# Kernel optimization log

Measured on AMD Instinct MI355X. Metric: run time of the kernel, lower is better.

## Reference

```python
import jax, jax.numpy as jnp
import numpy as np
from jax import lax

B, L = 8192, 64
N_VALUES, EMBED, HIDDEN, OUT = 1000, 64, 128, 128


def setup_inputs() -> dict:
    key = jax.random.key(0)
    ks = jax.random.split(key, 8)
    s = 0.1  # weight scale ~ 1/sqrt(hidden)
    return {
        "x": jax.random.randint(ks[0], (B, L), 0, N_VALUES),
        "embed": jax.random.normal(ks[1], (N_VALUES, EMBED), jnp.float32) * s,
        "W_ih": jax.random.normal(ks[2], (3 * HIDDEN, EMBED), jnp.float32) * s,
        "W_hh": jax.random.normal(ks[3], (3 * HIDDEN, HIDDEN), jnp.float32) * s,
        "b_ih": jax.random.normal(ks[4], (3 * HIDDEN,), jnp.float32) * s,
        "b_hh": jax.random.normal(ks[5], (3 * HIDDEN,), jnp.float32) * s,
        "W_out": jax.random.normal(ks[6], (OUT, HIDDEN), jnp.float32) * s,
        "b_out": jax.random.normal(ks[7], (OUT,), jnp.float32) * s,
    }


def _gru_encode(x, embed, W_ih, W_hh, b_ih, b_hh, W_out, b_out):
    e = embed[x]  # [B, L, E] embedding lookup
    H = W_hh.shape[1]
    # Precompute input-to-gate projections for all timesteps (batched GEMM).
    xg = jnp.einsum('ble,ge->blg', e, W_ih) + b_ih  # [B, L, 3H]

    def step(h, xg_t):
        hg = h @ W_hh.T + b_hh  # [B, 3H]
        xr, xz, xn = jnp.split(xg_t, 3, axis=-1)
        hr, hz, hn = jnp.split(hg, 3, axis=-1)
        r = jax.nn.sigmoid(xr + hr)
        z = jax.nn.sigmoid(xz + hz)
        n = jnp.tanh(xn + r * hn)  # PyTorch GRU: r gates the hidden 'new' term
        h_new = (1.0 - z) * n + z * h
        return h_new, None

    h0 = jnp.zeros((x.shape[0], H), e.dtype)
    h_last, _ = lax.scan(step, h0, jnp.swapaxes(xg, 0, 1))  # scan over time
    return h_last @ W_out.T + b_out  # [B, OUT]


def reference(x, embed, W_ih, W_hh, b_ih, b_hh, W_out, b_out):
    return _gru_encode(x, embed, W_ih, W_hh, b_ih, b_hh, W_out, b_out)
```

## Files before the change

kernel.cpp:

```cpp
#include <hip/hip_runtime.h>


typedef __bf16 bf16x8 __attribute__((ext_vector_type(8)));
typedef float  f32x4  __attribute__((ext_vector_type(4)));
typedef int    int4v  __attribute__((ext_vector_type(4)));
typedef unsigned int uint2v __attribute__((ext_vector_type(2)));

#define NV   1000
#define EMB  64
#define HD   128
#define G3   384
#define SEQ  64
#define BB   16

#define SC_RZ (-1.4426950408889634f)
#define SC_N  ( 2.8853900817779268f)

__device__ __forceinline__ float bflo(unsigned int word) {
    return __builtin_bit_cast(float, word << 16);
}
__device__ __forceinline__ float bfhi(unsigned int word) {
    return __builtin_bit_cast(float, word & 0xffff0000u);
}

__global__ void g_table_kernel(const float* __restrict__ embed,
                               const float* __restrict__ W_ih,
                               const float* __restrict__ b_ih,
                               const float* __restrict__ b_hh,
                               unsigned short* __restrict__ Gpk)
{
    __shared__ float emb[EMB];
    const int v = blockIdx.x;
    const int g = threadIdx.x;
    if (g < EMB) emb[g] = embed[v * EMB + g];
    __syncthreads();
    const float* wr = W_ih + g * EMB;
    float s = b_ih[g] + (g < 2 * HD ? b_hh[g] : 0.f);
    #pragma unroll
    for (int e = 0; e < EMB; e += 4) {
        const float4 w4 = *(const float4*)(wr + e);
        s += w4.x * emb[e] + w4.y * emb[e + 1] + w4.z * emb[e + 2] + w4.w * emb[e + 3];
    }
    const int hid = g & 127, gate = g >> 7;
    s *= (gate < 2) ? SC_RZ : SC_N;
    const int w8 = hid >> 4, c16i = hid & 15;
    Gpk[((v * 8 + w8) * 16 + c16i) * 4 + gate] =
        __builtin_bit_cast(unsigned short, (__bf16)s);
}

#define GRU_STEP(P, T)                                                             \
  {                                                                                \
    int4v tk = {0, 0, 0, 0};                                                       \
    if ((T) < SEQ - 1) tk = *(const int4v*)&xl[((T) + 1) * BB + quad * 4];         \
    f32x4 acc[3];                                                                  \
    float xn_[4];                                                                  \
    _Pragma("unroll") for (int j = 0; j < 4; ++j) {                                \
      acc[0][j] = bflo(pf[j][0]);                                         \
      acc[1][j] = bfhi(pf[j][0]);                                         \
      acc[2][j] = bnw;                                                    \
      xn_[j]    = bflo(pf[j][1]);                                         \
    }                                                                              \
    _Pragma("unroll") for (int ks = 0; ks < 4; ++ks) {                             \
      const bf16x8 af = *(const bf16x8*)(hbase + (P) * 4096 + aoff[ks]);           \
      _Pragma("unroll") for (int gate = 0; gate < 3; ++gate)                       \
        acc[gate] = __builtin_amdgcn_mfma_f32_16x16x32_bf16(                       \
            af, wf[gate][ks], acc[gate], 0, 0, 0);                                 \
    }                                                                              \
    if ((T) < SEQ - 1) {                                                           \
      _Pragma("unroll") for (int j = 0; j < 4; ++j)                                \
        pf[j] = *(const uint2v*)(gbase + (unsigned)(tk[j] * 1024 + goff));         \
    }                                                                              \
    _Pragma("unroll") for (int j = 0; j < 4; ++j) {                                \
      const float r  = __builtin_amdgcn_rcpf(                                      \
          1.f + __builtin_amdgcn_exp2f(acc[0][j]));                                \
      const float zg = __builtin_amdgcn_rcpf(                                      \
          1.f + __builtin_amdgcn_exp2f(acc[1][j]));                                \
      const float v  = __builtin_fmaf(r, acc[2][j], xn_[j]);                       \
      const float n  = __builtin_fmaf(-2.f,                                        \
          __builtin_amdgcn_rcpf(1.f + __builtin_amdgcn_exp2f(v)), 1.f);            \
      const float hn = __builtin_fmaf(zg, hreg[j] - n, n);                         \
      hreg[j] = hn;                                                                \
      *(unsigned short*)(hbase + (1 - (P)) * 4096 + woff[j]) =                     \
          __builtin_bit_cast(unsigned short, (__bf16)hn);                          \
    }                                                                              \
    asm volatile("s_waitcnt lgkmcnt(0)" ::: "memory");                             \
    __builtin_amdgcn_s_barrier();                                                  \
    __builtin_amdgcn_sched_barrier(0);                                             \
  }

__global__ __launch_bounds__(512, 4) void gru_kernel(
    const int*   __restrict__ x,    const unsigned short* __restrict__ Gpk,
    const float* __restrict__ Whh,  const float* __restrict__ bhh,
    const float* __restrict__ Wout, const float* __restrict__ bout,
    float* __restrict__ out)
{
    __shared__ unsigned short hA[2 * BB * HD];
    __shared__ int xl[SEQ * BB];

    const int tid  = threadIdx.x;
    const int lane = tid & 63;
    const int w    = tid >> 6;
    const int c16  = lane & 15;
    const int quad = lane >> 4;
    const int br0  = blockIdx.x * BB;

    #pragma unroll
    for (int i = 0; i < 2; ++i) {
        const int idx = i * 512 + tid;
        const int r = idx >> 6;
        const int t = idx & 63;
        xl[t * BB + r] = x[(br0 + r) * SEQ + t];
    }
    {
        unsigned int* hA32 = (unsigned int*)hA;
        #pragma unroll
        for (int i = 0; i < 2; ++i)
            hA32[i * 512 + tid] = 0u;
    }

    bf16x8 wf[3][4];
    #pragma unroll
    for (int gate = 0; gate < 3; ++gate)
    #pragma unroll
    for (int ks = 0; ks < 4; ++ks) {
        const float sc = (gate < 2) ? SC_RZ : SC_N;
        const int col = gate * HD + w * 16 + c16;
        const float* p = Whh + col * HD + ks * 32 + quad * 4;
        const float4 a = *(const float4*)p;
        const float4 b = *(const float4*)(p + 16);
        bf16x8 f;
        f[0] = (__bf16)(sc * a.x); f[1] = (__bf16)(sc * a.y);
        f[2] = (__bf16)(sc * a.z); f[3] = (__bf16)(sc * a.w);
        f[4] = (__bf16)(sc * b.x); f[5] = (__bf16)(sc * b.y);
        f[6] = (__bf16)(sc * b.z); f[7] = (__bf16)(sc * b.w);
        wf[gate][ks] = f;
    }

    const float bnw = SC_N * bhh[2 * HD + w * 16 + c16];

    int aoff[4];
    #pragma unroll
    for (int ks = 0; ks < 4; ++ks)
        aoff[ks] = c16 * 256 + ((ks * 64 + quad * 16) ^ ((c16 & 7) << 4));
    int woff[4];
    {
        const int hid  = w * 16 + c16;
        const int sidx = ((hid >> 5) << 5) | (((hid & 15) >> 2) << 3)
                       | (((hid >> 4) & 1) << 2) | (hid & 3);
        #pragma unroll
        for (int j = 0; j < 4; ++j) {
            const int row = quad * 4 + j;
            woff[j] = row * 256 + ((sidx * 2) ^ ((row & 7) << 4));
        }
    }

    char* hbase = (char*)hA;
    const char* gbase = (const char*)Gpk;
    const int goff = w * 128 + c16 * 8;

    float hreg[4] = {0.f, 0.f, 0.f, 0.f};
    const f32x4 z4 = {0.f, 0.f, 0.f, 0.f};

    __syncthreads();

    uint2v pf[4];
    {
        const int4v tk0 = *(const int4v*)&xl[0 * BB + quad * 4];
        #pragma unroll
        for (int j = 0; j < 4; ++j)
            pf[j] = *(const uint2v*)(gbase + (unsigned)(tk0[j] * 1024 + goff));
    }

    for (int tt = 0; tt < SEQ; tt += 2) {
        GRU_STEP(0, tt);
        GRU_STEP(1, tt + 1);
    }

    bf16x8 wo[4];
    #pragma unroll
    for (int ks = 0; ks < 4; ++ks) {
        const int col = w * 16 + c16;
        const float* p = Wout + col * HD + ks * 32 + quad * 4;
        const float4 a = *(const float4*)p;
        const float4 b = *(const float4*)(p + 16);
        bf16x8 f;
        f[0] = (__bf16)a.x; f[1] = (__bf16)a.y; f[2] = (__bf16)a.z; f[3] = (__bf16)a.w;
        f[4] = (__bf16)b.x; f[5] = (__bf16)b.y; f[6] = (__bf16)b.z; f[7] = (__bf16)b.w;
        wo[ks] = f;
    }
    const float bow = bout[w * 16 + c16];

    f32x4 oacc = z4;
    #pragma unroll
    for (int ks = 0; ks < 4; ++ks) {
        const bf16x8 af = *(const bf16x8*)(hbase + aoff[ks]);
        oacc = __builtin_amdgcn_mfma_f32_16x16x32_bf16(af, wo[ks], oacc, 0, 0, 0);
    }
    #pragma unroll
    for (int j = 0; j < 4; ++j) {
        const int row = br0 + quad * 4 + j;
        out[row * HD + w * 16 + c16] = oacc[j] + bow;
    }
}

extern "C" void kernel_launch(void* const* d_in, const int* in_sizes, int n_in,
                              void* d_out, int out_size, void* d_ws, size_t ws_size,
                              hipStream_t stream) {
    const int*   x     = (const int*)  d_in[0];
    const float* embed = (const float*)d_in[1];
    const float* W_ih  = (const float*)d_in[2];
    const float* W_hh  = (const float*)d_in[3];
    const float* b_ih  = (const float*)d_in[4];
    const float* b_hh  = (const float*)d_in[5];
    const float* W_out = (const float*)d_in[6];
    const float* b_out = (const float*)d_in[7];
    float* outp = (float*)d_out;
    unsigned short* Gpk = (unsigned short*)d_ws;

    const int Bsz = in_sizes[0] / SEQ;

    g_table_kernel<<<NV, G3, 0, stream>>>(embed, W_ih, b_ih, b_hh, Gpk);
    gru_kernel<<<Bsz / BB, 512, 0, stream>>>(x, Gpk, W_hh, b_hh, W_out, b_out, outp);
}
```

Baseline: 98.12 us.

## Interleave two 16-row batch groups per block to overlap MFMA with gate math

After: 99.77 us. About the same (+1.7%).

```diff
diff --git a/kernel.cpp b/kernel.cpp
--- a/kernel.cpp
+++ b/kernel.cpp
@@ -11,10 +11,13 @@
 #define HD   128
 #define G3   384
 #define SEQ  64
-#define BB   16
+#define BB   32
 
 #define SC_RZ (-1.4426950408889634f)
 #define SC_N  ( 2.8853900817779268f)
+
+#define EXP2F(x) __builtin_amdgcn_exp2f(x)
+#define RCPF(x)  __builtin_amdgcn_rcpf(x)
 
 __device__ __forceinline__ float bflo(unsigned int word) {
     return __builtin_bit_cast(float, word << 16);
@@ -48,53 +51,79 @@
         __builtin_bit_cast(unsigned short, (__bf16)s);
 }
 
-#define GRU_STEP(P, T)                                                             \
+#define GRU_PW(ACC, XN, HR, WBASE)                                                 \
+    _Pragma("unroll") for (int j = 0; j < 4; ++j) {                                \
+      const float r  = RCPF(1.f + EXP2F(ACC[0][j]));                               \
+      const float zg = RCPF(1.f + EXP2F(ACC[1][j]));                               \
+      const float v  = __builtin_fmaf(r, ACC[2][j], XN[j]);                        \
+      const float n  = __builtin_fmaf(-2.f, RCPF(1.f + EXP2F(v)), 1.f);            \
+      const float hn = __builtin_fmaf(zg, HR[j] - n, n);                           \
+      HR[j] = hn;                                                                  \
+      *(unsigned short*)((WBASE) + woff[j]) =                                      \
+          __builtin_bit_cast(unsigned short, (__bf16)hn);                          \
+    }
+
+#define PHASE_A(P, T)                                                              \
   {                                                                                \
-    int4v tk = {0, 0, 0, 0};                                                       \
-    if ((T) < SEQ - 1) tk = *(const int4v*)&xl[((T) + 1) * BB + quad * 4];         \
-    f32x4 acc[3];                                                                  \
-    float xn_[4];                                                                  \
+    int4v tkA = {0, 0, 0, 0};                                                      \
+    if ((T) < SEQ - 1) tkA = *(const int4v*)&xl[((T) + 1) * BB + quad * 4];        \
     _Pragma("unroll") for (int j = 0; j < 4; ++j) {                                \
-      acc[0][j] = bflo(pf[j][0]);                                         \
-      acc[1][j] = bfhi(pf[j][0]);                                         \
-      acc[2][j] = bnw;                                                    \
-      xn_[j]    = bflo(pf[j][1]);                                         \
+      accA[0][j] = bflo(pfA[j][0]);                                                \
+      accA[1][j] = bfhi(pfA[j][0]);                                                \
+      accA[2][j] = bnw;                                                            \
+      xnA[j]     = bflo(pfA[j][1]);                                                \
     }                                                                              \
     _Pragma("unroll") for (int ks = 0; ks < 4; ++ks) {                             \
       const bf16x8 af = *(const bf16x8*)(hbase + (P) * 4096 + aoff[ks]);           \
       _Pragma("unroll") for (int gate = 0; gate < 3; ++gate)                       \
-        acc[gate] = __builtin_amdgcn_mfma_f32_16x16x32_bf16(                       \
-            af, wf[gate][ks], acc[gate], 0, 0, 0);                                 \
+        accA[gate] = __builtin_amdgcn_mfma_f32_16x16x32_bf16(                      \
+            af, wf[gate][ks], accA[gate], 0, 0, 0);                                \
     }                                                                              \
     if ((T) < SEQ - 1) {                                                           \
       _Pragma("unroll") for (int j = 0; j < 4; ++j)                                \
-        pf[j] = *(const uint2v*)(gbase + (unsigned)(tk[j] * 1024 + goff));         \
-    }                                                                              \
-    _Pragma("unroll") for (int j = 0; j < 4; ++j) {                                \
-      const float r  = __builtin_amdgcn_rcpf(                                      \
-          1.f + __builtin_amdgcn_exp2f(acc[0][j]));                                \
-      const float zg = __builtin_amdgcn_rcpf(                                      \
-          1.f + __builtin_amdgcn_exp2f(acc[1][j]));                                \
-      const float v  = __builtin_fmaf(r, acc[2][j], xn_[j]);                       \
-      const float n  = __builtin_fmaf(-2.f,                                        \
-          __builtin_amdgcn_rcpf(1.f + __builtin_amdgcn_exp2f(v)), 1.f);            \
-      const float hn = __builtin_fmaf(zg, hreg[j] - n, n);                         \
-      hreg[j] = hn;                                                                \
-      *(unsigned short*)(hbase + (1 - (P)) * 4096 + woff[j]) =                     \
-          __builtin_bit_cast(unsigned short, (__bf16)hn);                          \
+        pfA[j] = *(const uint2v*)(gbase + (unsigned)(tkA[j] * 1024 + goff));       \
+    }                                                                              \
+    if ((T) > 0) {                                                                 \
+      GRU_PW(accB, xnB, hregB, hbase + 8192 + (P) * 4096)                          \
     }                                                                              \
     asm volatile("s_waitcnt lgkmcnt(0)" ::: "memory");                             \
     __builtin_amdgcn_s_barrier();                                                  \
     __builtin_amdgcn_sched_barrier(0);                                             \
   }
 
-__global__ __launch_bounds__(512, 4) void gru_kernel(
+#define PHASE_B(P, T)                                                              \
+  {                                                                                \
+    int4v tkB = {0, 0, 0, 0};                                                      \
+    if ((T) < SEQ - 1) tkB = *(const int4v*)&xl[((T) + 1) * BB + 16 + quad * 4];   \
+    _Pragma("unroll") for (int j = 0; j < 4; ++j) {                                \
+      accB[0][j] = bflo(pfB[j][0]);                                                \
+      accB[1][j] = bfhi(pfB[j][0]);                                                \
+      accB[2][j] = bnw;                                                            \
+      xnB[j]     = bflo(pfB[j][1]);                                                \
+    }                                                                              \
+    _Pragma("unroll") for (int ks = 0; ks < 4; ++ks) {                             \
+      const bf16x8 af = *(const bf16x8*)(hbase + 8192 + (P) * 4096 + aoff[ks]);    \
+      _Pragma("unroll") for (int gate = 0; gate < 3; ++gate)                       \
+        accB[gate] = __builtin_amdgcn_mfma_f32_16x16x32_bf16(                      \
+            af, wf[gate][ks], accB[gate], 0, 0, 0);                                \
+    }                                                                              \
+    if ((T) < SEQ - 1) {                                                           \
+      _Pragma("unroll") for (int j = 0; j < 4; ++j)                                \
+        pfB[j] = *(const uint2v*)(gbase + (unsigned)(tkB[j] * 1024 + goff));       \
+    }                                                                              \
+    GRU_PW(accA, xnA, hregA, hbase + (1 - (P)) * 4096)                             \
+    asm volatile("s_waitcnt lgkmcnt(0)" ::: "memory");                             \
+    __builtin_amdgcn_s_barrier();                                                  \
+    __builtin_amdgcn_sched_barrier(0);                                             \
+  }
+
+__global__ __launch_bounds__(512, 2) void gru_kernel(
     const int*   __restrict__ x,    const unsigned short* __restrict__ Gpk,
     const float* __restrict__ Whh,  const float* __restrict__ bhh,
     const float* __restrict__ Wout, const float* __restrict__ bout,
     float* __restrict__ out)
 {
-    __shared__ unsigned short hA[2 * BB * HD];
+    __shared__ unsigned short hA[2 * 2 * 16 * HD];
     __shared__ int xl[SEQ * BB];
 
     const int tid  = threadIdx.x;
@@ -105,7 +134,7 @@
     const int br0  = blockIdx.x * BB;
 
     #pragma unroll
-    for (int i = 0; i < 2; ++i) {
+    for (int i = 0; i < 4; ++i) {
         const int idx = i * 512 + tid;
         const int r = idx >> 6;
         const int t = idx & 63;
@@ -114,8 +143,10 @@
     {
         unsigned int* hA32 = (unsigned int*)hA;
         #pragma unroll
-        for (int i = 0; i < 2; ++i)
+        for (int i = 0; i < 2; ++i) {
             hA32[i * 512 + tid] = 0u;
+            hA32[2048 + i * 512 + tid] = 0u;
+        }
     }
 
     bf16x8 wf[3][4];
@@ -158,23 +189,38 @@
     const char* gbase = (const char*)Gpk;
     const int goff = w * 128 + c16 * 8;
 
-    float hreg[4] = {0.f, 0.f, 0.f, 0.f};
+    float hregA[4] = {0.f, 0.f, 0.f, 0.f};
+    float hregB[4] = {0.f, 0.f, 0.f, 0.f};
+    f32x4 accA[3], accB[3];
+    float xnA[4], xnB[4];
     const f32x4 z4 = {0.f, 0.f, 0.f, 0.f};
+    #pragma unroll
+    for (int g2 = 0; g2 < 3; ++g2) { accA[g2] = z4; accB[g2] = z4; }
+    #pragma unroll
+    for (int j = 0; j < 4; ++j) { xnA[j] = 0.f; xnB[j] = 0.f; }
 
     __syncthreads();
 
-    uint2v pf[4];
+    uint2v pfA[4], pfB[4];
     {
-        const int4v tk0 = *(const int4v*)&xl[0 * BB + quad * 4];
+        const int4v tA = *(const int4v*)&xl[0 * BB + quad * 4];
+        const int4v tB = *(const int4v*)&xl[0 * BB + 16 + quad * 4];
         #pragma unroll
         for (int j = 0; j < 4; ++j)
-            pf[j] = *(const uint2v*)(gbase + (unsigned)(tk0[j] * 1024 + goff));
+            pfA[j] = *(const uint2v*)(gbase + (unsigned)(tA[j] * 1024 + goff));
+        #pragma unroll
+        for (int j = 0; j < 4; ++j)
+            pfB[j] = *(const uint2v*)(gbase + (unsigned)(tB[j] * 1024 + goff));
     }
 
     for (int tt = 0; tt < SEQ; tt += 2) {
-        GRU_STEP(0, tt);
-        GRU_STEP(1, tt + 1);
-    }
+        PHASE_A(0, tt)
+        PHASE_B(0, tt)
+        PHASE_A(1, tt + 1)
+        PHASE_B(1, tt + 1)
+    }
+    GRU_PW(accB, xnB, hregB, hbase + 8192)
+    __syncthreads();
 
     bf16x8 wo[4];
     #pragma unroll
@@ -190,16 +236,19 @@
     }
     const float bow = bout[w * 16 + c16];
 
-    f32x4 oacc = z4;
+    f32x4 oaccA = z4, oaccB = z4;
     #pragma unroll
     for (int ks = 0; ks < 4; ++ks) {
-        const bf16x8 af = *(const bf16x8*)(hbase + aoff[ks]);
-        oacc = __builtin_amdgcn_mfma_f32_16x16x32_bf16(af, wo[ks], oacc, 0, 0, 0);
+        const bf16x8 afA = *(const bf16x8*)(hbase + aoff[ks]);
+        const bf16x8 afB = *(const bf16x8*)(hbase + 8192 + aoff[ks]);
+        oaccA = __builtin_amdgcn_mfma_f32_16x16x32_bf16(afA, wo[ks], oaccA, 0, 0, 0);
+        oaccB = __builtin_amdgcn_mfma_f32_16x16x32_bf16(afB, wo[ks], oaccB, 0, 0, 0);
     }
     #pragma unroll
     for (int j = 0; j < 4; ++j) {
         const int row = br0 + quad * 4 + j;
-        out[row * HD + w * 16 + c16] = oacc[j] + bow;
+        out[row * HD + w * 16 + c16] = oaccA[j] + bow;
+        out[(row + 16) * HD + w * 16 + c16] = oaccB[j] + bow;
     }
 }
 
```
